# Kernel optimization log

Measured on AMD Instinct MI355X. Metric: run time of the kernel, lower is better.

The kernel has to match this reference:

```python
import jax, jax.numpy as jnp
import numpy as np
import math

B, N, D_IN, D = 64, 1024, 128, 128

def setup_inputs() -> dict:
    key = jax.random.key(0)
    ks = jax.random.split(key, 8)
    s_in = 1.0 / math.sqrt(D_IN)
    inp = {
        "x": jax.random.normal(ks[0], (B, N, D_IN), dtype=jnp.float32),
        "valid_lens": jax.random.randint(ks[1], (B,), 1, N + 1, dtype=jnp.int32),
        "Wq": jax.random.uniform(ks[2], (D_IN, D), jnp.float32, -s_in, s_in),
        "bq": jax.random.uniform(ks[3], (D,), jnp.float32, -s_in, s_in),
        "Wk": jax.random.uniform(ks[4], (D_IN, D), jnp.float32, -s_in, s_in),
        "bk": jax.random.uniform(ks[5], (D,), jnp.float32, -s_in, s_in),
        "Wv": jax.random.uniform(ks[6], (D_IN, D), jnp.float32, -s_in, s_in),
        "bv": jax.random.uniform(ks[7], (D,), jnp.float32, -s_in, s_in),
    }
    return inp

def reference(x, valid_lens, Wq, bq, Wk, bk, Wv, bv):
    # QKV projections
    q = x @ Wq + bq  # [B, N, D]
    k = x @ Wk + bk
    v = x @ Wv + bv
    scores = jnp.einsum("bnd,bmd->bnm", q, k) / math.sqrt(D)  # [B, N, N]
    # mask[b, i, j] = True where i >= valid_len[b] or j >= valid_len[b]
    idx = jnp.arange(N)
    invalid = idx[None, :] >= valid_lens[:, None]            # [B, N]
    mask = invalid[:, :, None] | invalid[:, None, :]          # [B, N, N]
    scores_masked = jnp.where(mask, jnp.float32(-1e12), scores)
    attn = jax.nn.softmax(scores_masked, axis=-1)
    attn = attn * (1.0 - mask.astype(attn.dtype))             # zero masked entries/rows
    return jnp.einsum("bnm,bmd->bnd", attn, v)
```

## Files before the change

kernel.cpp:

```cpp
#include <hip/hip_runtime.h>
#include <hip/hip_bf16.h>
#include <stdint.h>

#define B_ 64
#define N_ 1024
#define D_ 128

typedef __attribute__((ext_vector_type(8))) short bf16x8;
typedef __attribute__((ext_vector_type(4))) float f32x4;

__device__ __forceinline__ unsigned short f2bf(float f) {
    union { float f; uint32_t u; } v; v.f = f;
    uint32_t u = v.u;
    return (unsigned short)((u + 0x7FFFu + ((u >> 16) & 1u)) >> 16);
}

__global__ __launch_bounds__(256) void wtrans_kernel(
    const float* __restrict__ Wq, const float* __restrict__ Wk,
    const float* __restrict__ Wv, unsigned short* __restrict__ wt)
{
    int p = blockIdx.x >> 4;
    int seg = blockIdx.x & 15;
    const float* W = (p == 0) ? Wq : (p == 1) ? Wk : Wv;
    unsigned short* dst = wt + p * (D_ * D_);
    for (int i = 0; i < 4; ++i) {
        int idx = seg * 1024 + i * 256 + (int)threadIdx.x;
        int k = idx >> 7, d = idx & 127;
        dst[d * D_ + k] = f2bf(W[idx]);
    }
}

__global__ __launch_bounds__(256) void proj_kernel(
    const float* __restrict__ x,
    const unsigned short* __restrict__ wtg,
    const float* __restrict__ bq, const float* __restrict__ bk,
    const float* __restrict__ bv,
    unsigned short* __restrict__ qo, unsigned short* __restrict__ ko,
    unsigned short* __restrict__ vto)
{
    __shared__ alignas(16) unsigned short xs[64 * 136];
    __shared__ alignas(16) unsigned short ws[128 * 136];
    const int tid = threadIdx.x;
    const int row0 = blockIdx.x * 64;

    for (int it = 0; it < 8; ++it) {
        int idx4 = it * 256 + tid;
        int r = idx4 >> 5, c4 = (idx4 & 31) * 4;
        const float4 v = *(const float4*)&x[(size_t)(row0 + r) * D_ + c4];
        unsigned short tmp[4] = { f2bf(v.x), f2bf(v.y), f2bf(v.z), f2bf(v.w) };
        *(uint2*)&xs[r * 136 + c4] = *(uint2*)tmp;
    }

    const int wave = tid >> 6, lane = tid & 63;
    const int lr = lane & 15, lg = lane >> 4;
    const f32x4 zero4 = {0.f, 0.f, 0.f, 0.f};

    for (int p = 0; p < 3; ++p) {
        __syncthreads();
        const unsigned short* wsrc = wtg + p * (D_ * D_);
        for (int it = 0; it < 8; ++it) {
            int idx8 = it * 256 + tid;
            int r = idx8 >> 4, c8 = (idx8 & 15) * 8;
            *(bf16x8*)&ws[r * 136 + c8] = *(const bf16x8*)&wsrc[idx8 * 8];
        }
        __syncthreads();

        bf16x8 a[4];
        for (int kk = 0; kk < 4; ++kk)
            a[kk] = *(const bf16x8*)&xs[(wave * 16 + lr) * 136 + kk * 32 + lg * 8];
        f32x4 acc[8];
        for (int nt = 0; nt < 8; ++nt) acc[nt] = zero4;
        for (int kk = 0; kk < 4; ++kk)
            for (int nt = 0; nt < 8; ++nt) {
                bf16x8 bfr = *(const bf16x8*)&ws[(nt * 16 + lr) * 136 + kk * 32 + lg * 8];
                acc[nt] = __builtin_amdgcn_mfma_f32_16x16x32_bf16(a[kk], bfr, acc[nt], 0, 0, 0);
            }

        if (p < 2) {
            const float* bias = (p == 0) ? bq : bk;
            unsigned short* outp = (p == 0) ? qo : ko;
            const float sc = (p == 0) ? 0.08838834764831845f : 1.0f;
            for (int nt = 0; nt < 8; ++nt) {
                int d = nt * 16 + lr;
                float bb = bias[d];
                for (int r = 0; r < 4; ++r) {
                    int grow = row0 + wave * 16 + lg * 4 + r;
                    outp[(size_t)grow * D_ + d] = f2bf((acc[nt][r] + bb) * sc);
                }
            }
        } else {
            __syncthreads();
            for (int nt = 0; nt < 8; ++nt) {
                int d = nt * 16 + lr;
                float bb = bv[d];
                for (int r = 0; r < 4; ++r)
                    ws[d * 72 + wave * 16 + lg * 4 + r] = f2bf(acc[nt][r] + bb);
            }
            __syncthreads();
            const int b = row0 >> 10, n0 = row0 & 1023;
            unsigned short* dst = vto + ((size_t)b * D_) * N_ + n0;
            for (int it = 0; it < 4; ++it) {
                int idx = it * 256 + tid;
                int d = idx >> 3, c8 = (idx & 7) * 8;
                *(bf16x8*)&dst[(size_t)d * N_ + c8] = *(const bf16x8*)&ws[d * 72 + c8];
            }
        }
    }
}

__global__ __launch_bounds__(512, 2) void attn_kernel(
    const unsigned short* __restrict__ qg, const unsigned short* __restrict__ kg,
    const unsigned short* __restrict__ vtg, const int* __restrict__ valid_lens,
    float* __restrict__ out, int* __restrict__ ctr)
{
    __shared__ alignas(16) unsigned short smem[54272];
    __shared__ int slot;

    const int tid = threadIdx.x;
    const int wave = tid >> 6, lane = tid & 63;
    const int lr = lane & 15, lg = lane >> 4;
    const int grp = tid >> 8;
    const int wg = wave & 3;
    const int t256 = tid & 255;
    const int k_r = t256 >> 4, k_c = (t256 & 15) * 8;
    const int v_d = t256 >> 3, v_c = (t256 & 7) * 8;
    unsigned short* const ks_my = smem + grp * 8704;
    unsigned short* const vt_my = smem + 17408 + grp * 9216;
    unsigned short* const pw    = smem + 35840 + wave * 2304;
    float* const cmbO = (float*)smem;
    float* const cmbL = ((float*)smem) + 16640;
    const f32x4 zero4 = {0.f, 0.f, 0.f, 0.f};

    int item = blockIdx.x;
    while (item < 512) {
        const int qt = 7 - (item >> 6);
        const int b  = item & 63;
        const int L  = valid_lens[b];
        const int q0 = qt * 128;
        float* outb = out + ((size_t)b * N_ + q0) * D_;

        if (q0 >= L) {
            #pragma unroll
            for (int it = 0; it < 8; ++it) {
                int idx4 = it * 512 + tid;
                int r = idx4 >> 5, c4 = (idx4 & 31) * 4;
                float4 z; z.x = z.y = z.z = z.w = 0.f;
                *(float4*)&outb[(size_t)r * D_ + c4] = z;
            }
        } else {
            const int ntiles = (L + 63) >> 6;
            const int H = (ntiles + 1) >> 1;
            const int myStart = grp ? H : 0;
            const int myCnt = grp ? (ntiles - H) : H;
            const unsigned short* kgb = kg + (size_t)b * N_ * D_;
            const unsigned short* vtb = vtg + (size_t)b * D_ * N_;

            bf16x8 aq[2][4];
            #pragma unroll
            for (int rt = 0; rt < 2; ++rt) {
                const unsigned short* qrow =
                    qg + ((size_t)b * N_ + q0 + wg * 32 + rt * 16 + lr) * D_;
                #pragma unroll
                for (int kk = 0; kk < 4; ++kk)
                    aq[rt][kk] = *(const bf16x8*)&qrow[kk * 32 + lg * 8];
            }

            f32x4 oacc[2][8];
            #pragma unroll
            for (int rt = 0; rt < 2; ++rt)
                #pragma unroll
                for (int i = 0; i < 8; ++i) oacc[rt][i] = zero4;
            float lsum[2] = {0.f, 0.f};

            bf16x8 kreg[4], vreg[4];

            if (myCnt > 0) {
                const int kv0 = myStart * 64;
                #pragma unroll
                for (int it = 0; it < 4; ++it)
                    kreg[it] = *(const bf16x8*)&kgb[(size_t)(kv0 + it * 16 + k_r) * D_ + k_c];
                #pragma unroll
                for (int it = 0; it < 4; ++it)
                    vreg[it] = *(const bf16x8*)&vtb[(size_t)(it * 32 + v_d) * N_ + kv0 + v_c];
                #pragma unroll
                for (int it = 0; it < 4; ++it)
                    *(bf16x8*)&ks_my[(it * 16 + k_r) * 136 + k_c] = kreg[it];
                #pragma unroll
                for (int it = 0; it < 4; ++it)
                    *(bf16x8*)&vt_my[(it * 32 + v_d) * 72 + v_c] = vreg[it];
            }
            __syncthreads();

            for (int r = 0; r < H; ++r) {
                const bool valid = (r < myCnt);
                const int t = myStart + r;
                const int kv0 = t * 64;

                if (r + 1 < myCnt) {
                    const int kvn = kv0 + 64;
                    #pragma unroll
                    for (int it = 0; it < 4; ++it)
                        kreg[it] = *(const bf16x8*)&kgb[(size_t)(kvn + it * 16 + k_r) * D_ + k_c];
                    #pragma unroll
                    for (int it = 0; it < 4; ++it)
                        vreg[it] = *(const bf16x8*)&vtb[(size_t)(it * 32 + v_d) * N_ + kvn + v_c];
                    __builtin_amdgcn_sched_barrier(0);
                }

                if (valid) {
                    f32x4 s[2][4];
                    #pragma unroll
                    for (int nt = 0; nt < 4; ++nt) {
                        s[0][nt] = zero4; s[1][nt] = zero4;
                        #pragma unroll
                        for (int kk = 0; kk < 4; ++kk) {
                            bf16x8 bk_ = *(const bf16x8*)&ks_my[(nt * 16 + lr) * 136 + kk * 32 + lg * 8];
                            s[0][nt] = __builtin_amdgcn_mfma_f32_16x16x32_bf16(bk_, aq[0][kk], s[0][nt], 0, 0, 0);
                            s[1][nt] = __builtin_amdgcn_mfma_f32_16x16x32_bf16(bk_, aq[1][kk], s[1][nt], 0, 0, 0);
                        }
                    }
                    #pragma unroll
                    for (int nt = 0; nt < 4; ++nt) {
                        const int kvb = kv0 + nt * 16 + lg * 4;
                        #pragma unroll
                        for (int rt = 0; rt < 2; ++rt) {
                            float e0 = (kvb + 0 < L) ? __expf(s[rt][nt][0]) : 0.f;
                            float e1 = (kvb + 1 < L) ? __expf(s[rt][nt][1]) : 0.f;
                            float e2 = (kvb + 2 < L) ? __expf(s[rt][nt][2]) : 0.f;
                            float e3 = (kvb + 3 < L) ? __expf(s[rt][nt][3]) : 0.f;
                            lsum[rt] += (e0 + e1) + (e2 + e3);
                            uint2 wv;
                            wv.x = (uint32_t)f2bf(e0) | ((uint32_t)f2bf(e1) << 16);
                            wv.y = (uint32_t)f2bf(e2) | ((uint32_t)f2bf(e3) << 16);
                            *(uint2*)&pw[(rt * 16 + lr) * 72 + nt * 16 + lg * 4] = wv;
                        }
                    }
                    #pragma unroll
                    for (int kk = 0; kk < 2; ++kk) {
                        bf16x8 ap0 = *(const bf16x8*)&pw[(0 * 16 + lr) * 72 + kk * 32 + lg * 8];
                        bf16x8 ap1 = *(const bf16x8*)&pw[(1 * 16 + lr) * 72 + kk * 32 + lg * 8];
                        #pragma unroll
                        for (int nt = 0; nt < 8; ++nt) {
                            bf16x8 bv_ = *(const bf16x8*)&vt_my[(nt * 16 + lr) * 72 + kk * 32 + lg * 8];
                            oacc[0][nt] = __builtin_amdgcn_mfma_f32_16x16x32_bf16(ap0, bv_, oacc[0][nt], 0, 0, 0);
                            oacc[1][nt] = __builtin_amdgcn_mfma_f32_16x16x32_bf16(ap1, bv_, oacc[1][nt], 0, 0, 0);
                        }
                    }
                }
                __syncthreads();
                if (r + 1 < myCnt) {
                    #pragma unroll
                    for (int it = 0; it < 4; ++it)
                        *(bf16x8*)&ks_my[(it * 16 + k_r) * 136 + k_c] = kreg[it];
                    #pragma unroll
                    for (int it = 0; it < 4; ++it)
                        *(bf16x8*)&vt_my[(it * 32 + v_d) * 72 + v_c] = vreg[it];
                }
                __syncthreads();
            }

            #pragma unroll
            for (int rt = 0; rt < 2; ++rt) {
                float l = lsum[rt];
                l += __shfl_xor(l, 16);
                l += __shfl_xor(l, 32);
                lsum[rt] = l;
            }

            if (grp == 1) {
                #pragma unroll
                for (int rt = 0; rt < 2; ++rt) {
                    if (lg == 0) cmbL[wg * 32 + rt * 16 + lr] = lsum[rt];
                    #pragma unroll
                    for (int r2 = 0; r2 < 4; ++r2) {
                        const int row = wg * 32 + rt * 16 + lg * 4 + r2;
                        #pragma unroll
                        for (int nt = 0; nt < 8; ++nt)
                            cmbO[row * 130 + nt * 16 + lr] = oacc[rt][nt][r2];
                    }
                }
            }
            __syncthreads();
            if (grp == 0) {
                #pragma unroll
                for (int rt = 0; rt < 2; ++rt) {
                    const int qrow = q0 + wg * 32 + rt * 16 + lr;
                    float tot = lsum[rt] + cmbL[wg * 32 + rt * 16 + lr];
                    float invq = (qrow < L) ? 1.0f / tot : 0.0f;
                    #pragma unroll
                    for (int r2 = 0; r2 < 4; ++r2) {
                        const float invr = __shfl(invq, lg * 4 + r2);
                        const int row = wg * 32 + rt * 16 + lg * 4 + r2;
                        #pragma unroll
                        for (int nt = 0; nt < 8; ++nt) {
                            const int col = nt * 16 + lr;
                            outb[(size_t)row * D_ + col] =
                                (oacc[rt][nt][r2] + cmbO[row * 130 + col]) * invr;
                        }
                    }
                }
            }
            __syncthreads();
        }

        if (tid == 0) slot = 256 + atomicAdd(ctr, 1);
        __syncthreads();
        item = slot;
        __syncthreads();
    }
}

extern "C" void kernel_launch(void* const* d_in, const int* in_sizes, int n_in,
                              void* d_out, int out_size, void* d_ws, size_t ws_size,
                              hipStream_t stream) {
    const float* x    = (const float*)d_in[0];
    const int*   vlen = (const int*)d_in[1];
    const float* Wq   = (const float*)d_in[2];
    const float* bq   = (const float*)d_in[3];
    const float* Wk   = (const float*)d_in[4];
    const float* bk   = (const float*)d_in[5];
    const float* Wv   = (const float*)d_in[6];
    const float* bv   = (const float*)d_in[7];
    float* out = (float*)d_out;

    unsigned short* wt  = (unsigned short*)d_ws;
    unsigned short* qws = (unsigned short*)((char*)d_ws + 98304);
    unsigned short* kws = qws + (size_t)B_ * N_ * D_;
    unsigned short* vtws = kws + (size_t)B_ * N_ * D_;
    int* ctr = (int*)((char*)d_ws + 98304 + 3 * (size_t)B_ * N_ * D_ * 2);

    hipMemsetAsync(ctr, 0, 4, stream);
    wtrans_kernel<<<48, 256, 0, stream>>>(Wq, Wk, Wv, wt);
    proj_kernel<<<(B_ * N_) / 64, 256, 0, stream>>>(x, wt, bq, bk, bv, qws, kws, vtws);
    attn_kernel<<<256, 512, 0, stream>>>(qws, kws, vtws, vlen, out, ctr);
}
```

Measured before the change: 72.48 us.

## Double-buffer K/V tiles, pass P via lane shuffles, drop memset launch

The attention loop now keeps two LDS buffers for K and V^T, so each tile is written into the alternate buffer and one of the two barriers per iteration goes away. The exp'd probabilities are rearranged into MFMA A-operand layout with cross-lane shuffles instead of a round trip through a per-wave LDS scratch area. MFMA sections are wrapped in s_setprio. The counter reset moves from hipMemsetAsync into the weight-transpose kernel, removing one launch. LDS use rises from about 106 KB to 140 KB per block, which could cut the two-blocks-per-CU occupancy that launch_bounds asks for.

```diff
diff --git a/kernel.cpp b/kernel.cpp
--- a/kernel.cpp
+++ b/kernel.cpp
@@ -17,8 +17,10 @@
 
 __global__ __launch_bounds__(256) void wtrans_kernel(
     const float* __restrict__ Wq, const float* __restrict__ Wk,
-    const float* __restrict__ Wv, unsigned short* __restrict__ wt)
+    const float* __restrict__ Wv, unsigned short* __restrict__ wt,
+    int* __restrict__ ctr)
 {
+    if (blockIdx.x == 0 && threadIdx.x == 0) ctr[0] = 0;
     int p = blockIdx.x >> 4;
     int seg = blockIdx.x & 15;
     const float* W = (p == 0) ? Wq : (p == 1) ? Wk : Wv;
@@ -113,7 +115,7 @@
     const unsigned short* __restrict__ vtg, const int* __restrict__ valid_lens,
     float* __restrict__ out, int* __restrict__ ctr)
 {
-    __shared__ alignas(16) unsigned short smem[54272];
+    __shared__ alignas(16) unsigned short smem[71680];
     __shared__ int slot;
 
     const int tid = threadIdx.x;
@@ -124,12 +126,15 @@
     const int t256 = tid & 255;
     const int k_r = t256 >> 4, k_c = (t256 & 15) * 8;
     const int v_d = t256 >> 3, v_c = (t256 & 7) * 8;
-    unsigned short* const ks_my = smem + grp * 8704;
-    unsigned short* const vt_my = smem + 17408 + grp * 9216;
-    unsigned short* const pw    = smem + 35840 + wave * 2304;
+    unsigned short* const ks_b[2] = { smem + grp * 17408,
+                                      smem + grp * 17408 + 8704 };
+    unsigned short* const vt_b[2] = { smem + 34816 + grp * 18432,
+                                      smem + 34816 + grp * 18432 + 9216 };
     float* const cmbO = (float*)smem;
     float* const cmbL = ((float*)smem) + 16640;
     const f32x4 zero4 = {0.f, 0.f, 0.f, 0.f};
+    const bool hbit = (lg >> 1) != 0;
+    const bool mbit = (lg & 1) != 0;
 
     int item = blockIdx.x;
     while (item < 512) {
@@ -184,17 +189,18 @@
                     vreg[it] = *(const bf16x8*)&vtb[(size_t)(it * 32 + v_d) * N_ + kv0 + v_c];
                 #pragma unroll
                 for (int it = 0; it < 4; ++it)
-                    *(bf16x8*)&ks_my[(it * 16 + k_r) * 136 + k_c] = kreg[it];
+                    *(bf16x8*)&ks_b[0][(it * 16 + k_r) * 136 + k_c] = kreg[it];
                 #pragma unroll
                 for (int it = 0; it < 4; ++it)
-                    *(bf16x8*)&vt_my[(it * 32 + v_d) * 72 + v_c] = vreg[it];
+                    *(bf16x8*)&vt_b[0][(it * 32 + v_d) * 72 + v_c] = vreg[it];
             }
             __syncthreads();
 
             for (int r = 0; r < H; ++r) {
                 const bool valid = (r < myCnt);
-                const int t = myStart + r;
-                const int kv0 = t * 64;
+                const int kv0 = (myStart + r) * 64;
+                unsigned short* const ks_my = ks_b[r & 1];
+                unsigned short* const vt_my = vt_b[r & 1];
 
                 if (r + 1 < myCnt) {
                     const int kvn = kv0 + 64;
@@ -209,6 +215,7 @@
 
                 if (valid) {
                     f32x4 s[2][4];
+                    __builtin_amdgcn_s_setprio(1);
                     #pragma unroll
                     for (int nt = 0; nt < 4; ++nt) {
                         s[0][nt] = zero4; s[1][nt] = zero4;
@@ -219,6 +226,9 @@
                             s[1][nt] = __builtin_amdgcn_mfma_f32_16x16x32_bf16(bk_, aq[1][kk], s[1][nt], 0, 0, 0);
                         }
                     }
+                    __builtin_amdgcn_s_setprio(0);
+
+                    uint32_t pwv[2][8];
                     #pragma unroll
                     for (int nt = 0; nt < 4; ++nt) {
                         const int kvb = kv0 + nt * 16 + lg * 4;
@@ -229,32 +239,67 @@
                             float e2 = (kvb + 2 < L) ? __expf(s[rt][nt][2]) : 0.f;
                             float e3 = (kvb + 3 < L) ? __expf(s[rt][nt][3]) : 0.f;
                             lsum[rt] += (e0 + e1) + (e2 + e3);
-                            uint2 wv;
-                            wv.x = (uint32_t)f2bf(e0) | ((uint32_t)f2bf(e1) << 16);
-                            wv.y = (uint32_t)f2bf(e2) | ((uint32_t)f2bf(e3) << 16);
-                            *(uint2*)&pw[(rt * 16 + lr) * 72 + nt * 16 + lg * 4] = wv;
-                        }
-                    }
-                    #pragma unroll
-                    for (int kk = 0; kk < 2; ++kk) {
-                        bf16x8 ap0 = *(const bf16x8*)&pw[(0 * 16 + lr) * 72 + kk * 32 + lg * 8];
-                        bf16x8 ap1 = *(const bf16x8*)&pw[(1 * 16 + lr) * 72 + kk * 32 + lg * 8];
-                        #pragma unroll
-                        for (int nt = 0; nt < 8; ++nt) {
-                            bf16x8 bv_ = *(const bf16x8*)&vt_my[(nt * 16 + lr) * 72 + kk * 32 + lg * 8];
-                            oacc[0][nt] = __builtin_amdgcn_mfma_f32_16x16x32_bf16(ap0, bv_, oacc[0][nt], 0, 0, 0);
-                            oacc[1][nt] = __builtin_amdgcn_mfma_f32_16x16x32_bf16(ap1, bv_, oacc[1][nt], 0, 0, 0);
-                        }
-                    }
-                }
-                __syncthreads();
+                            pwv[rt][nt * 2 + 0] = (uint32_t)f2bf(e0) | ((uint32_t)f2bf(e1) << 16);
+                            pwv[rt][nt * 2 + 1] = (uint32_t)f2bf(e2) | ((uint32_t)f2bf(e3) << 16);
+                        }
+                    }
+
+                    #pragma unroll
+                    for (int rt = 0; rt < 2; ++rt) {
+                        uint32_t sh[4], so[4];
+                        #pragma unroll
+                        for (int i = 0; i < 4; ++i) {
+                            int i0 = (i >> 1) * 4 + (i & 1);
+                            sh[i] = hbit ? pwv[rt][i0 + 2] : pwv[rt][i0];
+                            so[i] = hbit ? pwv[rt][i0] : pwv[rt][i0 + 2];
+                        }
+                        uint32_t rv[4];
+                        #pragma unroll
+                        for (int i = 0; i < 4; ++i)
+                            rv[i] = __shfl_xor((int)so[i], 32);
+                        const bool c2 = (hbit != mbit);
+                        uint32_t s2[4], kp[4];
+                        #pragma unroll
+                        for (int i = 0; i < 4; ++i) {
+                            s2[i] = c2 ? sh[i] : rv[i];
+                            kp[i] = c2 ? rv[i] : sh[i];
+                        }
+                        uint32_t r2v[4];
+                        #pragma unroll
+                        for (int i = 0; i < 4; ++i)
+                            r2v[i] = __shfl_xor((int)s2[i], 16);
+                        uint32_t apw[2][4];
+                        #pragma unroll
+                        for (int kk = 0; kk < 2; ++kk)
+                            #pragma unroll
+                            for (int c = 0; c < 2; ++c) {
+                                uint32_t kw = kp[kk * 2 + c], rw = r2v[kk * 2 + c];
+                                apw[kk][c]     = mbit ? rw : kw;
+                                apw[kk][2 + c] = mbit ? kw : rw;
+                            }
+                        __builtin_amdgcn_s_setprio(1);
+                        #pragma unroll
+                        for (int kk = 0; kk < 2; ++kk) {
+                            bf16x8 ap = *(bf16x8*)&apw[kk][0];
+                            #pragma unroll
+                            for (int nt = 0; nt < 8; ++nt) {
+                                bf16x8 bv_ = *(const bf16x8*)&vt_my[(nt * 16 + lr) * 72 + kk * 32 + lg * 8];
+                                oacc[rt][nt] = __builtin_amdgcn_mfma_f32_16x16x32_bf16(ap, bv_, oacc[rt][nt], 0, 0, 0);
+                            }
+                        }
+                        __builtin_amdgcn_s_setprio(0);
+                    }
+                }
+
                 if (r + 1 < myCnt) {
+                    unsigned short* const ks_nx = ks_b[(r + 1) & 1];
+                    unsigned short* const vt_nx = vt_b[(r + 1) & 1];
                     #pragma unroll
                     for (int it = 0; it < 4; ++it)
-                        *(bf16x8*)&ks_my[(it * 16 + k_r) * 136 + k_c] = kreg[it];
+                        *(bf16x8*)&ks_nx[(it * 16 + k_r) * 136 + k_c] = kreg[it];
                     #pragma unroll
                     for (int it = 0; it < 4; ++it)
-                        *(bf16x8*)&vt_my[(it * 32 + v_d) * 72 + v_c] = vreg[it];
+                        *(bf16x8*)&vt_nx[(it * 32 + v_d) * 72 + v_c] = vreg[it];
                 }
                 __syncthreads();
             }
@@ -329,8 +374,7 @@
     unsigned short* vtws = kws + (size_t)B_ * N_ * D_;
     int* ctr = (int*)((char*)d_ws + 98304 + 3 * (size_t)B_ * N_ * D_ * 2);
 
-    hipMemsetAsync(ctr, 0, 4, stream);
-    wtrans_kernel<<<48, 256, 0, stream>>>(Wq, Wk, Wv, wt);
+    wtrans_kernel<<<48, 256, 0, stream>>>(Wq, Wk, Wv, wt, ctr);
     proj_kernel<<<(B_ * N_) / 64, 256, 0, stream>>>(x, wt, bq, bk, bv, qws, kws, vtws);
     attn_kernel<<<256, 512, 0, stream>>>(qws, kws, vtws, vlen, out, ctr);
 }
```

New measurement: 82.20 us. 13.4% more time.
